# Performance work log

Hardware: AMD Instinct MI355X
Metric: run time of the kernel (lower is better)

Reference implementation:

```python
import jax, jax.numpy as jnp
import numpy as np

HEADS = 16
DIM_HEAD = 64
QUERY_DIM = 1024


def setup_inputs() -> dict:
    key = jax.random.key(0)
    ks = jax.random.split(key, 5)
    B, S, D = 4, 2048, QUERY_DIM
    inner = HEADS * DIM_HEAD
    s = 0.02
    return {
        "x": jax.random.normal(ks[0], (B, S, D), dtype=jnp.float32),
        "Wq": jax.random.normal(ks[1], (D, inner), dtype=jnp.float32) * s,
        "Wk": jax.random.normal(ks[2], (D, inner), dtype=jnp.float32) * s,
        "Wv": jax.random.normal(ks[3], (D, inner), dtype=jnp.float32) * s,
        "Wo": jax.random.normal(ks[4], (inner, D), dtype=jnp.float32) * s,
    }


def reference(x, Wq, Wk, Wv, Wo):
    B, S, D = x.shape
    h, d = HEADS, DIM_HEAD
    scale = d ** (-0.5)
    # projections -> [B, h, S, d]
    q = (x @ Wq).reshape(B, S, h, d).transpose(0, 2, 1, 3)
    k = (x @ Wk).reshape(B, S, h, d).transpose(0, 2, 1, 3)
    v = (x @ Wv).reshape(B, S, h, d).transpose(0, 2, 1, 3)
    # scores [B, h, S, S]
    attn = jnp.einsum("bhqd,bhkd->bhqk", q, k) * scale
    attn = jax.nn.softmax(attn, axis=-1)
    out = jnp.einsum("bhqk,bhkd->bhqd", attn, v)
    out = out.transpose(0, 2, 1, 3).reshape(B, S, h * d)
    return out @ Wo
```

## Files before the change

### kernel.cpp

```cpp
#include <hip/hip_runtime.h>
#include <cstddef>

#define BATCH  4
#define SLEN   2048
#define NHEADS 16
#define DHEAD  64
#define DMODEL 1024

typedef __attribute__((ext_vector_type(8)))  short short8;
typedef __attribute__((ext_vector_type(4)))  float f32x4;
typedef __attribute__((ext_vector_type(16))) float f32x16;

__device__ inline unsigned short f2bf(float f) {
    union { float f; unsigned int u; } v; v.f = f;
    unsigned int r = v.u + 0x7fffu + ((v.u >> 16) & 1u);
    return (unsigned short)(r >> 16);
}

__device__ inline float fast_exp2(float x) {
#if __has_builtin(__builtin_amdgcn_exp2f)
    return __builtin_amdgcn_exp2f(x);
#else
    return __expf(x * 0.69314718f);
#endif
}

__device__ inline void gload_lds16(const unsigned short* g, unsigned short* l) {
    __builtin_amdgcn_global_load_lds(
        (const __attribute__((address_space(1))) void*)g,
        (__attribute__((address_space(3))) void*)l, 16, 0, 0);
}

__global__ __launch_bounds__(256)
void prep(const float* __restrict__ x, unsigned short* __restrict__ xb,
          const float* __restrict__ W0, const float* __restrict__ W1,
          const float* __restrict__ W2, const float* __restrict__ W3,
          unsigned short* __restrict__ T0, unsigned short* __restrict__ T1,
          unsigned short* __restrict__ T2, unsigned short* __restrict__ T3)
{
    __shared__ unsigned short T[64 * 72];
    const int bid = blockIdx.x;
    const int tid = threadIdx.x;

    if (bid < 4096) {
        const int i = bid * 256 + tid;
        const float4 a = ((const float4*)x)[2 * i];
        const float4 b = ((const float4*)x)[2 * i + 1];
        short8 o;
        o[0] = (short)f2bf(a.x); o[1] = (short)f2bf(a.y);
        o[2] = (short)f2bf(a.z); o[3] = (short)f2bf(a.w);
        o[4] = (short)f2bf(b.x); o[5] = (short)f2bf(b.y);
        o[6] = (short)f2bf(b.z); o[7] = (short)f2bf(b.w);
        ((short8*)xb)[i] = o;
        return;
    }

    const int idx = bid - 4096;
    const int z = idx >> 8;
    const float* W = (z == 0) ? W0 : (z == 1) ? W1 : (z == 2) ? W2 : W3;
    unsigned short* Wt = (z == 0) ? T0 : (z == 1) ? T1 : (z == 2) ? T2 : T3;
    const int n0 = (idx & 15) * 64, k0 = ((idx >> 4) & 15) * 64;

    #pragma unroll
    for (int it = 0; it < 2; it++) {
        const int t2 = it * 256 + tid;
        const int row = t2 >> 3, col8 = (t2 & 7) * 8;
        const float4 a = *(const float4*)(W + (size_t)(k0 + row) * DMODEL + n0 + col8);
        const float4 b = *(const float4*)(W + (size_t)(k0 + row) * DMODEL + n0 + col8 + 4);
        short8 o;
        o[0] = (short)f2bf(a.x); o[1] = (short)f2bf(a.y);
        o[2] = (short)f2bf(a.z); o[3] = (short)f2bf(a.w);
        o[4] = (short)f2bf(b.x); o[5] = (short)f2bf(b.y);
        o[6] = (short)f2bf(b.z); o[7] = (short)f2bf(b.w);
        *(short8*)&T[row * 72 + col8] = o;
    }
    __syncthreads();
    #pragma unroll
    for (int it = 0; it < 2; it++) {
        const int t2 = it * 256 + tid;
        const int nn = t2 >> 3, k8 = (t2 & 7) * 8;
        short8 v;
        #pragma unroll
        for (int j = 0; j < 8; j++) v[j] = (short)T[(k8 + j) * 72 + nn];
        *(short8*)(Wt + (size_t)(n0 + nn) * DMODEL + k0 + k8) = v;
    }
}

template<int KIND>
__global__ __launch_bounds__(256)
void gemm_bf16(const unsigned short* __restrict__ A,
               const unsigned short* __restrict__ B0,
               const unsigned short* __restrict__ B1,
               const unsigned short* __restrict__ B2,
               void* __restrict__ C0v, void* __restrict__ C1v, void* __restrict__ C2v)
{
    constexpr int N = DMODEL, K = DMODEL;
    __shared__ unsigned short lds[17408];
    unsigned short* As = lds;
    unsigned short* Bs = lds + 8192;

    const int z = blockIdx.z;
    const unsigned short* Bw = (z == 0) ? B0 : (z == 1) ? B1 : B2;
    void* Cv = (z == 0) ? C0v : (z == 1) ? C1v : C2v;

    const int tid  = threadIdx.x;
    const int lane = tid & 63;
    const int wave = tid >> 6;
    const int c  = lane & 15, qd = lane >> 4;
    const int wr = wave >> 1, wc = wave & 1;
    const int m0 = blockIdx.y * 128, n0 = blockIdx.x * 128;

    const unsigned short* ag[4];
    const unsigned short* bg[4];
    unsigned short* al[4];
    unsigned short* bl[4];
    #pragma unroll
    for (int j = 0; j < 4; j++) {
        const int cid = j * 256 + tid;
        const int row = cid >> 3;
        const int k8  = (cid & 7) ^ (row & 7);
        ag[j] = A  + (size_t)(m0 + row) * K + k8 * 8;
        bg[j] = Bw + (size_t)(n0 + row) * K + k8 * 8;
        al[j] = &As[cid * 8];
        bl[j] = &Bs[cid * 8];
    }

    f32x4 acc[4][4];
    #pragma unroll
    for (int mb = 0; mb < 4; mb++)
        #pragma unroll
        for (int nb = 0; nb < 4; nb++)
            #pragma unroll
            for (int r = 0; r < 4; r++) acc[mb][nb][r] = 0.f;

    for (int k0 = 0; k0 < K; k0 += 64) {
        __syncthreads();
        #pragma unroll
        for (int j = 0; j < 4; j++) {
            gload_lds16(ag[j], al[j]);
            gload_lds16(bg[j], bl[j]);
            ag[j] += 64; bg[j] += 64;
        }
        __syncthreads();

        #pragma unroll
        for (int ks = 0; ks < 2; ks++) {
            const int sw = (ks * 4 + qd) ^ (c & 7);
            short8 af[4], bf[4];
            #pragma unroll
            for (int mb = 0; mb < 4; mb++)
                af[mb] = *(const short8*)&As[((wr * 64 + mb * 16 + c) * 8 + sw) * 8];
            #pragma unroll
            for (int nb = 0; nb < 4; nb++)
                bf[nb] = *(const short8*)&Bs[((wc * 64 + nb * 16 + c) * 8 + sw) * 8];
            #pragma unroll
            for (int mb = 0; mb < 4; mb++)
                #pragma unroll
                for (int nb = 0; nb < 4; nb++)
                    acc[mb][nb] = __builtin_amdgcn_mfma_f32_16x16x32_bf16(
                        af[mb], bf[nb], acc[mb][nb], 0, 0, 0);
        }
    }

    const int mbase = m0 + wr * 64 + qd * 4;
    const int nbase = n0 + wc * 64 + c;
    if (KIND == 1) {
        float* C = (float*)Cv;
        #pragma unroll
        for (int mb = 0; mb < 4; mb++)
            #pragma unroll
            for (int nb = 0; nb < 4; nb++)
                #pragma unroll
                for (int r = 0; r < 4; r++)
                    C[(size_t)(mbase + mb * 16 + r) * N + nbase + nb * 16] = acc[mb][nb][r];
    } else if (z != 2) {
        unsigned short* C = (unsigned short*)Cv;
        const float osc = (z == 0) ? 0.18033688f : 1.0f;
        #pragma unroll
        for (int mb = 0; mb < 4; mb++)
            #pragma unroll
            for (int nb = 0; nb < 4; nb++)
                #pragma unroll
                for (int r = 0; r < 4; r++)
                    C[(size_t)(mbase + mb * 16 + r) * N + nbase + nb * 16] =
                        f2bf(acc[mb][nb][r] * osc);
    } else {
        __syncthreads();
        unsigned short* T = lds;
        #pragma unroll
        for (int mb = 0; mb < 4; mb++) {
            const int sl = wr * 64 + qd * 4 + mb * 16;
            #pragma unroll
            for (int nb = 0; nb < 4; nb++) {
                const int dl = wc * 64 + nb * 16 + c;
                ushort4 val = make_ushort4(f2bf(acc[mb][nb][0]), f2bf(acc[mb][nb][1]),
                                           f2bf(acc[mb][nb][2]), f2bf(acc[mb][nb][3]));
                *(ushort4*)&T[dl * 136 + sl] = val;
            }
        }
        __syncthreads();
        unsigned short* C = (unsigned short*)Cv;
        const int b  = m0 >> 11;
        const int s0 = m0 & 2047;
        #pragma unroll
        for (int it = 0; it < 8; it++) {
            const int chunk = it * 256 + tid;
            const int row  = chunk >> 4;
            const int col8 = (chunk & 15) * 8;
            const int n = n0 + row;
            const int h2 = n >> 6, dd = n & 63;
            short8 v = *(const short8*)&T[row * 136 + col8];
            *(short8*)(C + ((size_t)((b * 16 + h2) * 64 + dd)) * SLEN + s0 + col8) = v;
        }
    }
}

__global__ __launch_bounds__(256, 4)
void attn_mfma6(const unsigned short* __restrict__ qb,
                const unsigned short* __restrict__ kb,
                const unsigned short* __restrict__ vtb,
                unsigned short* __restrict__ O)
{
    __shared__ unsigned short lds[18432];
    unsigned short* Ks = lds;
    unsigned short* Vs = lds + 4096;

    const int tid = threadIdx.x;
    const int w   = tid >> 6, ln = tid & 63;
    const int c5  = ln & 31;
    const int l5i = ln >> 5;

    const int L  = blockIdx.x + (int)gridDim.x * blockIdx.y;
    const int wg = (L & 7) * 128 + (L >> 3);
    const int qt = wg & 15, bh = wg >> 4;
    const int b = bh >> 4, h = bh & 15;
    const size_t bh_base = ((size_t)b * SLEN * NHEADS + h) * 64;
    constexpr int RS = NHEADS * 64;

    const int srow = ln >> 3;
    const int sk8  = (ln & 7) ^ srow;
    const int prow = (srow & 3) | ((w & 1) << 2) | (((srow >> 2) & 1) << 3) | ((w >> 1) << 4);
    const unsigned short* kg0 = kb + bh_base + (size_t)prow * RS + sk8 * 8;
    const unsigned short* kg1 = kg0 + (size_t)32 * RS;
    const unsigned short* vg0 = vtb + ((size_t)bh * 64 + w * 8 + srow) * SLEN + sk8 * 8;
    const unsigned short* vg1 = vg0 + (size_t)32 * SLEN;
    unsigned short* kl0 = &Ks[(w * 64 + ln) * 8];
    unsigned short* kl1 = kl0 + 2048;
    unsigned short* vl0 = &Vs[(w * 64 + ln) * 8];
    unsigned short* vl1 = vl0 + 2048;

    const int qtile = qt * 128 + w * 32;

    short8 qf[4];
    #pragma unroll
    for (int kst = 0; kst < 4; kst++)
        qf[kst] = *(const short8*)(qb + bh_base +
            (size_t)(qtile + c5) * RS + kst * 16 + l5i * 8);

    f32x16 acc[2];
    #pragma unroll
    for (int db = 0; db < 2; db++)
        #pragma unroll
        for (int r = 0; r < 16; r++) acc[db][r] = 0.f;
    float lsum = 0.f;
    const int cl7 = c5 & 7;

    for (int kt = 0; kt < SLEN / 64; kt++) {
        __syncthreads();
        gload_lds16(kg0, kl0); gload_lds16(kg1, kl1);
        gload_lds16(vg0, vl0); gload_lds16(vg1, vl1);
        kg0 += (size_t)64 * RS; kg1 += (size_t)64 * RS; vg0 += 64; vg1 += 64;
        __syncthreads();

        #pragma unroll
        for (int kb32 = 0; kb32 < 2; kb32++) {
            f32x16 sacc;
            #pragma unroll
            for (int r = 0; r < 16; r++) sacc[r] = 0.f;
            __builtin_amdgcn_s_setprio(1);
            #pragma unroll
            for (int kst = 0; kst < 4; kst++) {
                const int slot = (kst * 2 + l5i) ^ cl7;
                short8 kf = *(const short8*)&Ks[((kb32 * 32 + c5) * 8 + slot) * 8];
                sacc = __builtin_amdgcn_mfma_f32_32x32x16_bf16(
                    kf, qf[kst], sacc, 0, 0, 0);
            }
            __builtin_amdgcn_s_setprio(0);

            unsigned pk[8];
            {
                float p[16];
                float s0 = 0.f, s1 = 0.f;
                #pragma unroll
                for (int r = 0; r < 16; r += 2) {
                    p[r]     = fast_exp2(sacc[r]);
                    p[r + 1] = fast_exp2(sacc[r + 1]);
                    s0 += p[r]; s1 += p[r + 1];
                }
                lsum += s0 + s1;
                #pragma unroll
                for (int i = 0; i < 8; i++)
                    pk[i] = __builtin_amdgcn_perm(
                        __float_as_uint(p[2 * i + 1]), __float_as_uint(p[2 * i]),
                        0x07060302u);
            }

            #pragma unroll
            for (int kk = 0; kk < 2; kk++) {
                const int k2 = kb32 * 2 + kk;
                union { unsigned u[4]; short8 s; } t;
                t.u[0] = pk[4 * kk + 0];
                t.u[1] = pk[4 * kk + 1];
                t.u[2] = pk[4 * kk + 2];
                t.u[3] = pk[4 * kk + 3];
                const short8 pf = t.s;
                __builtin_amdgcn_s_setprio(1);
                #pragma unroll
                for (int db = 0; db < 2; db++) {
                    const int slot = (k2 * 2 + l5i) ^ cl7;
                    short8 vf = *(const short8*)&Vs[((db * 32 + c5) * 8 + slot) * 8];
                    acc[db] = __builtin_amdgcn_mfma_f32_32x32x16_bf16(
                        vf, pf, acc[db], 0, 0, 0);
                }
                __builtin_amdgcn_s_setprio(0);
            }
        }
    }

    __syncthreads();
    float l = lsum;
    l += __shfl_xor(l, 32);
    const float inv = 1.001953125f / l;
    unsigned short* E = lds + w * 2304;
    #pragma unroll
    for (int db = 0; db < 2; db++)
        #pragma unroll
        for (int u = 0; u < 4; u++) {
            const int d0 = db * 32 + 8 * u + 4 * l5i;
            const int q  = c5;
            ushort4 val = make_ushort4(
                f2bf(acc[db][4 * u + 0] * inv),
                f2bf(acc[db][4 * u + 1] * inv),
                f2bf(acc[db][4 * u + 2] * inv),
                f2bf(acc[db][4 * u + 3] * inv));
            *(ushort4*)&E[q * 72 + d0] = val;
        }
    __builtin_amdgcn_wave_barrier();
    #pragma unroll
    for (int it = 0; it < 4; it++) {
        const int t2 = it * 64 + ln;
        const int row = t2 >> 3, col8 = (t2 & 7) * 8;
        short8 o = *(const short8*)&E[row * 72 + col8];
        *(short8*)(O + bh_base + (size_t)(qtile + row) * RS + col8) = o;
    }
}

extern "C" void kernel_launch(void* const* d_in, const int* in_sizes, int n_in,
                              void* d_out, int out_size, void* d_ws, size_t ws_size,
                              hipStream_t stream)
{
    const float* x  = (const float*)d_in[0];
    const float* Wq = (const float*)d_in[1];
    const float* Wk = (const float*)d_in[2];
    const float* Wv = (const float*)d_in[3];
    const float* Wo = (const float*)d_in[4];
    float* out = (float*)d_out;

    const size_t per = (size_t)BATCH * SLEN * NHEADS * DHEAD;
    const size_t wsz = (size_t)DMODEL * DMODEL;
    unsigned short* qb  = (unsigned short*)d_ws;
    unsigned short* kb  = qb  + per;
    unsigned short* vtb = kb  + per;
    unsigned short* xb  = vtb + per;
    unsigned short* wtq = xb  + per;
    unsigned short* wtk = wtq + wsz;
    unsigned short* wtv = wtk + wsz;
    unsigned short* wto = wtv + wsz;

    dim3 blk(256);
    prep<<<dim3(4096 + 1024), blk, 0, stream>>>(x, xb, Wq, Wk, Wv, Wo,
                                                wtq, wtk, wtv, wto);

    gemm_bf16<0><<<dim3(8, 64, 3), blk, 0, stream>>>(xb, wtq, wtk, wtv, qb, kb, vtb);

    attn_mfma6<<<dim3(SLEN / 128, BATCH * NHEADS), blk, 0, stream>>>(qb, kb, vtb, qb);

    gemm_bf16<1><<<dim3(8, 64, 1), blk, 0, stream>>>(qb, wto, wto, wto, out, out, out);
}
```

Measured before the change: 262.6 us.

## Replace QKV projection with 256x256-tile 8-wave pipelined fused GEMM

The QKV projection becomes one 512-thread kernel with 256x256 output tiles over a concatenated weight matrix (wtq/wtk/wtv treated as one N=3072 B). It double-buffers A and B through LDS with direct global-to-LDS loads, interleaves the fragment reads with MFMA phases under s_setprio, and swizzles block order for cache locality. The goal is higher arithmetic intensity and better latency hiding than the previous 128x128 tile kernel. V is now written transposed directly from registers as ushort4, with no LDS staging. This relies on the three weight buffers being contiguous in the workspace and adds heavy register pressure.

```diff
diff --git a/kernel.cpp b/kernel.cpp
--- a/kernel.cpp
+++ b/kernel.cpp
@@ -29,6 +29,10 @@
     __builtin_amdgcn_global_load_lds(
         (const __attribute__((address_space(1))) void*)g,
         (__attribute__((address_space(3))) void*)l, 16, 0, 0);
+}
+
+__device__ inline void barrier_fence() {
+    asm volatile("s_barrier" ::: "memory");
 }
 
 __global__ __launch_bounds__(256)
@@ -86,22 +90,186 @@
     }
 }
 
-template<int KIND>
+__global__ __launch_bounds__(512, 2)
+void gemm8p_qkv(const unsigned short* __restrict__ A,
+                const unsigned short* __restrict__ Bw,
+                unsigned short* __restrict__ qb,
+                unsigned short* __restrict__ kb,
+                unsigned short* __restrict__ vtb)
+{
+    constexpr int K = DMODEL;
+    constexpr int NT = K / 64;
+    __shared__ unsigned short lds8[65536];
+
+    const int tid  = threadIdx.x;
+    const int lane = tid & 63;
+    const int wave = tid >> 6;
+    const int c  = lane & 15, qd = lane >> 4;
+    const int wr = wave >> 2, wc = wave & 3;
+    const int cl7 = c & 7;
+
+    const int flat = blockIdx.y * 12 + blockIdx.x;
+    const int swz  = (flat & 7) * 48 + (flat >> 3);
+    const int bx = swz % 12, by = swz / 12;
+    const int n0 = bx * 256, m0 = by * 256;
+
+    const unsigned short* ag[4];
+    const unsigned short* bg[4];
+    int lo[4];
+    #pragma unroll
+    for (int j = 0; j < 4; j++) {
+        const int cid = j * 512 + tid;
+        const int row = cid >> 3;
+        const int k8  = (cid & 7) ^ (row & 7);
+        ag[j] = A  + (size_t)(m0 + row) * K + k8 * 8;
+        bg[j] = Bw + (size_t)(n0 + row) * K + k8 * 8;
+        lo[j] = cid * 8;
+    }
+
+#define STAGE_A(bufi) { _Pragma("unroll") \
+    for (int j = 0; j < 4; j++) { \
+        gload_lds16(ag[j], &lds8[(bufi) * 16384 + lo[j]]); ag[j] += 64; } }
+#define STAGE_B(bufi) { _Pragma("unroll") \
+    for (int j = 0; j < 4; j++) { \
+        gload_lds16(bg[j], &lds8[32768 + (bufi) * 16384 + lo[j]]); bg[j] += 64; } }
+
+    f32x4 acc[8][4];
+    #pragma unroll
+    for (int mb = 0; mb < 8; mb++)
+        #pragma unroll
+        for (int nb = 0; nb < 4; nb++)
+            #pragma unroll
+            for (int r = 0; r < 4; r++) acc[mb][nb][r] = 0.f;
+
+    STAGE_A(0); STAGE_B(0); STAGE_B(1);
+
+    short8 bf[4], af[4];
+
+    for (int t = 0; t < NT; t++) {
+        const int buf = t & 1;
+        const unsigned short* Asb = &lds8[buf * 16384];
+        const unsigned short* Bsb = &lds8[32768 + buf * 16384];
+
+        if (t + 1 < NT) STAGE_A(buf ^ 1);
+        if (t == NT - 1) asm volatile("s_waitcnt vmcnt(0)" ::: "memory");
+        else             asm volatile("s_waitcnt vmcnt(8)" ::: "memory");
+        barrier_fence();
+        {
+            const int sw = qd ^ cl7;
+            #pragma unroll
+            for (int nb = 0; nb < 4; nb++)
+                bf[nb] = *(const short8*)&Bsb[((wc * 64 + nb * 16 + c) * 8 + sw) * 8];
+            #pragma unroll
+            for (int mb = 0; mb < 4; mb++)
+                af[mb] = *(const short8*)&Asb[((wr * 128 + mb * 16 + c) * 8 + sw) * 8];
+        }
+        __builtin_amdgcn_s_setprio(1);
+        #pragma unroll
+        for (int mb = 0; mb < 4; mb++)
+            #pragma unroll
+            for (int nb = 0; nb < 4; nb++)
+                acc[mb][nb] = __builtin_amdgcn_mfma_f32_16x16x32_bf16(
+                    af[mb], bf[nb], acc[mb][nb], 0, 0, 0);
+        __builtin_amdgcn_s_setprio(0);
+        barrier_fence();
+
+        {
+            const int sw = qd ^ cl7;
+            #pragma unroll
+            for (int mb = 0; mb < 4; mb++)
+                af[mb] = *(const short8*)&Asb[((wr * 128 + (mb + 4) * 16 + c) * 8 + sw) * 8];
+        }
+        barrier_fence();
+        __builtin_amdgcn_s_setprio(1);
+        #pragma unroll
+        for (int mb = 0; mb < 4; mb++)
+            #pragma unroll
+            for (int nb = 0; nb < 4; nb++)
+                acc[mb + 4][nb] = __builtin_amdgcn_mfma_f32_16x16x32_bf16(
+                    af[mb], bf[nb], acc[mb + 4][nb], 0, 0, 0);
+        __builtin_amdgcn_s_setprio(0);
+        barrier_fence();
+
+        {
+            const int sw = (4 + qd) ^ cl7;
+            #pragma unroll
+            for (int nb = 0; nb < 4; nb++)
+                bf[nb] = *(const short8*)&Bsb[((wc * 64 + nb * 16 + c) * 8 + sw) * 8];
+            #pragma unroll
+            for (int mb = 0; mb < 4; mb++)
+                af[mb] = *(const short8*)&Asb[((wr * 128 + mb * 16 + c) * 8 + sw) * 8];
+        }
+        barrier_fence();
+        __builtin_amdgcn_s_setprio(1);
+        #pragma unroll
+        for (int mb = 0; mb < 4; mb++)
+            #pragma unroll
+            for (int nb = 0; nb < 4; nb++)
+                acc[mb][nb] = __builtin_amdgcn_mfma_f32_16x16x32_bf16(
+                    af[mb], bf[nb], acc[mb][nb], 0, 0, 0);
+        __builtin_amdgcn_s_setprio(0);
+        barrier_fence();
+
+        {
+            const int sw = (4 + qd) ^ cl7;
+            #pragma unroll
+            for (int mb = 0; mb < 4; mb++)
+                af[mb] = *(const short8*)&Asb[((wr * 128 + (mb + 4) * 16 + c) * 8 + sw) * 8];
+        }
+        if (t + 2 < NT) STAGE_B(buf);
+        barrier_fence();
+        __builtin_amdgcn_s_setprio(1);
+        #pragma unroll
+        for (int mb = 0; mb < 4; mb++)
+            #pragma unroll
+            for (int nb = 0; nb < 4; nb++)
+                acc[mb + 4][nb] = __builtin_amdgcn_mfma_f32_16x16x32_bf16(
+                    af[mb], bf[nb], acc[mb + 4][nb], 0, 0, 0);
+        __builtin_amdgcn_s_setprio(0);
+        barrier_fence();
+    }
+#undef STAGE_A
+#undef STAGE_B
+
+    const int z = bx >> 2;
+    const int ncol0 = (n0 & 1023) + wc * 64;
+    const int mbase = m0 + wr * 128 + qd * 4;
+    if (z != 2) {
+        unsigned short* C = z ? kb : qb;
+        const float sc = z ? 1.0f : 0.18033688f;
+        #pragma unroll
+        for (int mb = 0; mb < 8; mb++)
+            #pragma unroll
+            for (int nb = 0; nb < 4; nb++)
+                #pragma unroll
+                for (int r = 0; r < 4; r++)
+                    C[(size_t)(mbase + mb * 16 + r) * DMODEL + ncol0 + nb * 16 + c] =
+                        f2bf(acc[mb][nb][r] * sc);
+    } else {
+        #pragma unroll
+        for (int mb = 0; mb < 8; mb++) {
+            const int row = mbase + mb * 16;
+            const int b = row >> 11, s = row & 2047;
+            #pragma unroll
+            for (int nb = 0; nb < 4; nb++) {
+                const int n_in = ncol0 + nb * 16 + c;
+                const int h = n_in >> 6, dd = n_in & 63;
+                ushort4 val = make_ushort4(f2bf(acc[mb][nb][0]), f2bf(acc[mb][nb][1]),
+                                           f2bf(acc[mb][nb][2]), f2bf(acc[mb][nb][3]));
+                *(ushort4*)(vtb + ((size_t)((b * 16 + h) * 64 + dd)) * SLEN + s) = val;
+            }
+        }
+    }
+}
+
 __global__ __launch_bounds__(256)
-void gemm_bf16(const unsigned short* __restrict__ A,
-               const unsigned short* __restrict__ B0,
-               const unsigned short* __restrict__ B1,
-               const unsigned short* __restrict__ B2,
-               void* __restrict__ C0v, void* __restrict__ C1v, void* __restrict__ C2v)
+void gemm_fin(const unsigned short* __restrict__ A,
+              const unsigned short* __restrict__ Bw,
+              float* __restrict__ C)
 {
     constexpr int N = DMODEL, K = DMODEL;
-    __shared__ unsigned short lds[17408];
-    unsigned short* As = lds;
-    unsigned short* Bs = lds + 8192;
-
-    const int z = blockIdx.z;
-    const unsigned short* Bw = (z == 0) ? B0 : (z == 1) ? B1 : B2;
-    void* Cv = (z == 0) ? C0v : (z == 1) ? C1v : C2v;
+    __shared__ unsigned short As[128 * 64];
+    __shared__ unsigned short Bs[128 * 64];
 
     const int tid  = threadIdx.x;
     const int lane = tid & 63;
@@ -164,55 +332,13 @@
 
     const int mbase = m0 + wr * 64 + qd * 4;
     const int nbase = n0 + wc * 64 + c;
-    if (KIND == 1) {
-        float* C = (float*)Cv;
-        #pragma unroll
-        for (int mb = 0; mb < 4; mb++)
-            #pragma unroll
-            for (int nb = 0; nb < 4; nb++)
-                #pragma unroll
-                for (int r = 0; r < 4; r++)
-                    C[(size_t)(mbase + mb * 16 + r) * N + nbase + nb * 16] = acc[mb][nb][r];
-    } else if (z != 2) {
-        unsigned short* C = (unsigned short*)Cv;
-        const float osc = (z == 0) ? 0.18033688f : 1.0f;
-        #pragma unroll
-        for (int mb = 0; mb < 4; mb++)
-            #pragma unroll
-            for (int nb = 0; nb < 4; nb++)
-                #pragma unroll
-                for (int r = 0; r < 4; r++)
-                    C[(size_t)(mbase + mb * 16 + r) * N + nbase + nb * 16] =
-                        f2bf(acc[mb][nb][r] * osc);
-    } else {
-        __syncthreads();
-        unsigned short* T = lds;
-        #pragma unroll
-        for (int mb = 0; mb < 4; mb++) {
-            const int sl = wr * 64 + qd * 4 + mb * 16;
-            #pragma unroll
-            for (int nb = 0; nb < 4; nb++) {
-                const int dl = wc * 64 + nb * 16 + c;
-                ushort4 val = make_ushort4(f2bf(acc[mb][nb][0]), f2bf(acc[mb][nb][1]),
-                                           f2bf(acc[mb][nb][2]), f2bf(acc[mb][nb][3]));
-                *(ushort4*)&T[dl * 136 + sl] = val;
-            }
-        }
-        __syncthreads();
-        unsigned short* C = (unsigned short*)Cv;
-        const int b  = m0 >> 11;
-        const int s0 = m0 & 2047;
-        #pragma unroll
-        for (int it = 0; it < 8; it++) {
-            const int chunk = it * 256 + tid;
-            const int row  = chunk >> 4;
-            const int col8 = (chunk & 15) * 8;
-            const int n = n0 + row;
-            const int h2 = n >> 6, dd = n & 63;
-            short8 v = *(const short8*)&T[row * 136 + col8];
-            *(short8*)(C + ((size_t)((b * 16 + h2) * 64 + dd)) * SLEN + s0 + col8) = v;
-        }
-    }
+    #pragma unroll
+    for (int mb = 0; mb < 4; mb++)
+        #pragma unroll
+        for (int nb = 0; nb < 4; nb++)
+            #pragma unroll
+            for (int r = 0; r < 4; r++)
+                C[(size_t)(mbase + mb * 16 + r) * N + nbase + nb * 16] = acc[mb][nb][r];
 }
 
 __global__ __launch_bounds__(256, 4)
@@ -381,9 +507,9 @@
     prep<<<dim3(4096 + 1024), blk, 0, stream>>>(x, xb, Wq, Wk, Wv, Wo,
                                                 wtq, wtk, wtv, wto);
 
-    gemm_bf16<0><<<dim3(8, 64, 3), blk, 0, stream>>>(xb, wtq, wtk, wtv, qb, kb, vtb);
+    gemm8p_qkv<<<dim3(12, 32), dim3(512), 0, stream>>>(xb, wtq, qb, kb, vtb);
 
     attn_mfma6<<<dim3(SLEN / 128, BATCH * NHEADS), blk, 0, stream>>>(qb, kb, vtb, qb);
 
-    gemm_bf16<1><<<dim3(8, 64, 1), blk, 0, stream>>>(qb, wto, wto, wto, out, out, out);
-}
+    gemm_fin<<<dim3(8, 64), blk, 0, stream>>>(qb, wto, out);
+}
```

New measurement: 267.1 us. No clear change (+1.7%).
